# Optimization experiments

Measured on AMD Instinct MI355X. Metric: run time of the kernel, lower is better.

Reference implementation:

```python
import jax, jax.numpy as jnp
import numpy as np

N = 50_000          # nodes
E = 1_600_000       # edges (avg degree 32)
IN = 128            # in_feats
H = 4               # num_heads
F = 32              # out_feats per head
CUTOFF = 4.0        # bessel_cutoff
P = 7               # envelope_exponent + 1
ENV_A = -(P + 1) * (P + 2) / 2.0   # -36
ENV_B = P * (P + 2)                # 63
ENV_C = -P * (P + 1) / 2.0         # -28


def setup_inputs() -> dict:
    key = jax.random.key(0)
    ks = jax.random.split(key, 8)
    x = jax.random.normal(ks[0], (N, IN), dtype=jnp.float32)
    distance = jax.random.uniform(ks[1], (E,), dtype=jnp.float32) * CUTOFF
    W_src = jax.random.normal(ks[2], (H * F, IN), dtype=jnp.float32) * 0.05
    b_src = jnp.zeros((H * F,), dtype=jnp.float32)
    W_dst = jax.random.normal(ks[3], (H * F, IN), dtype=jnp.float32) * 0.05
    b_dst = jnp.zeros((H * F,), dtype=jnp.float32)
    attn = jax.random.normal(ks[4], (1, H, F), dtype=jnp.float32) * 0.1
    prelu_alpha = jnp.full((H,), 0.25, dtype=jnp.float32)
    frequencies = jnp.arange(1.0, H + 1.0, dtype=jnp.float32) * np.pi
    src = jax.random.randint(ks[5], (E,), 0, N, dtype=jnp.int32)
    dst = jax.random.randint(ks[6], (E,), 0, N, dtype=jnp.int32)
    return dict(x=x, distance=distance, W_src=W_src, b_src=b_src,
                W_dst=W_dst, b_dst=b_dst, attn=attn,
                prelu_alpha=prelu_alpha, frequencies=frequencies,
                src=src, dst=dst)


def _bessel_coeff(distance, frequencies):
    # distance: [E] -> d_scaled: [E,1]; frequencies: [H] -> coeff: [E,H]
    d = (distance / CUTOFF)[:, None]
    d_p0 = d ** P
    env = d + ENV_A * d_p0 + ENV_B * (d_p0 * d) + ENV_C * (d_p0 * d * d)
    return env * jnp.sin(frequencies * d)


def reference(x, distance, W_src, b_src, W_dst, b_dst, attn,
              prelu_alpha, frequencies, src, dst):
    n = x.shape[0]
    feat_src = (x @ W_src.T + b_src).reshape(n, H, F)   # [N,H,F]
    feat_dst = (x @ W_dst.T + b_dst).reshape(n, H, F)   # [N,H,F]

    coeff = _bessel_coeff(distance, frequencies)[:, :, None]  # [E,H,1]

    el = feat_src[src]                                  # [E,H,F] gather
    e = (el + feat_dst[dst]) * coeff                    # u_add_v then bessel scale
    e = jnp.where(e >= 0, e, prelu_alpha[None, :, None] * e)  # PReLU per head
    score = jnp.einsum('ehf,hf->eh', e, attn[0])        # [E,H]

    # edge softmax over incoming edges per dst node, per head
    seg_max = jax.ops.segment_max(score, dst, num_segments=n)        # [N,H]
    ex = jnp.exp(score - seg_max[dst])                               # [E,H]
    denom = jax.ops.segment_sum(ex, dst, num_segments=n)             # [N,H]
    a = ex / denom[dst]                                              # [E,H]

    # u_mul_e + scatter-sum aggregation
    msgs = el * a[:, :, None]                                        # [E,H,F]
    rst = jax.ops.segment_sum(msgs, dst, num_segments=n)             # [N,H,F]
    return rst
```

## Files before the change

### kernel.cpp

```cpp
#include <hip/hip_runtime.h>
#include <hip/hip_bf16.h>
#include <math.h>

#define N_NODES 50000
#define E_EDGES 1600000
#define HF 128
#define INV_CUTOFF 0.25f
#define ENV_A -36.0f
#define ENV_B 63.0f
#define ENV_C -28.0f

#define GEMM_BLOCKS ((N_NODES + 63) / 64)
#define REC_CAP 72
#define NBUCK 196
#define BUCK_CAP 8960
#define EPB 6250
#define SPLIT 4
#define LCAP 32

typedef __attribute__((ext_vector_type(8))) short bf16x8;
typedef __attribute__((ext_vector_type(4))) float f32x4;

__device__ __forceinline__ unsigned short f2bf(float f) {
  unsigned u = __float_as_uint(f);
  u += 0x7fffu + ((u >> 16) & 1u);
  return (unsigned short)(u >> 16);
}
__device__ __forceinline__ unsigned pack2(float lo, float hi) {
  return (unsigned)f2bf(lo) | ((unsigned)f2bf(hi) << 16);
}
__device__ __forceinline__ float2 up2(unsigned v) {
  return make_float2(__uint_as_float(v << 16), __uint_as_float(v & 0xffff0000u));
}

__device__ __forceinline__ float2 pk_add(float2 a, float2 b) {
  float2 d;
  asm("v_pk_add_f32 %0, %1, %2" : "=v"(d) : "v"(a), "v"(b));
  return d;
}
__device__ __forceinline__ float2 pk_fma(float2 a, float2 b, float2 c) {
  float2 d;
  asm("v_pk_fma_f32 %0, %1, %2, %3" : "=v"(d) : "v"(a), "v"(b), "v"(c));
  return d;
}
__device__ __forceinline__ float2 pk_abs(float2 a) {
  float2 d;
  d.x = __uint_as_float(__float_as_uint(a.x) & 0x7fffffffu);
  d.y = __uint_as_float(__float_as_uint(a.y) & 0x7fffffffu);
  return d;
}

__global__ void prep_w(const float* __restrict__ Ws, const float* __restrict__ Wd,
                       unsigned short* __restrict__ wbf) {
  const int q = blockIdx.x * 256 + threadIdx.x;
  if (q < 4096) {
    const int n = q >> 4, c = q & 15;
    const float* Wp = ((n < 128) ? Ws : Wd) + (size_t)(n & 127) * HF + c * 8;
    const float4 v0 = *(const float4*)Wp;
    const float4 v1 = *(const float4*)(Wp + 4);
    uint4 pk;
    pk.x = pack2(v0.x, v0.y); pk.y = pack2(v0.z, v0.w);
    pk.z = pack2(v1.x, v1.y); pk.w = pack2(v1.z, v1.w);
    *(uint4*)(wbf + (size_t)n * HF + ((c ^ (n & 15)) * 8)) = pk;
  }
}

__global__ __launch_bounds__(256) void feat_gemm(
    const float* __restrict__ x, const unsigned short* __restrict__ wbf,
    const float* __restrict__ bs, const float* __restrict__ bd,
    unsigned short* __restrict__ fs, float* __restrict__ fd) {
  __shared__ unsigned short wlds[256 * 128];

  for (int i = threadIdx.x; i < 4096; i += 256)
    ((uint4*)wlds)[i] = ((const uint4*)wbf)[i];

  const int lane = threadIdx.x & 63;
  const int wave = threadIdx.x >> 6;
  const int m = lane & 15;
  const int quad = lane >> 4;
  const int m0 = blockIdx.x * 64 + wave * 16;
  const int row = m0 + m;
  const int rowc = (row < N_NODES) ? row : (N_NODES - 1);

  union { bf16x8 v; unsigned u[4]; } af[4];
  #pragma unroll
  for (int kt = 0; kt < 4; kt++) {
    const float* xp = x + (size_t)rowc * HF + kt * 32 + quad * 8;
    const float4 u0 = *(const float4*)xp;
    const float4 u1 = *(const float4*)(xp + 4);
    af[kt].u[0] = pack2(u0.x, u0.y); af[kt].u[1] = pack2(u0.z, u0.w);
    af[kt].u[2] = pack2(u1.x, u1.y); af[kt].u[3] = pack2(u1.z, u1.w);
  }

  __syncthreads();

  float accA[16][4];
  #pragma unroll
  for (int nt = 0; nt < 16; nt++) {
    const int nrow = nt * 16 + m;
    f32x4 acc = {0.f, 0.f, 0.f, 0.f};
    #pragma unroll
    for (int kt = 0; kt < 4; kt++) {
      const int pc = (kt * 4 + quad) ^ m;
      const bf16x8 bf = *(const bf16x8*)(wlds + (size_t)nrow * HF + pc * 8);
      acc = __builtin_amdgcn_mfma_f32_16x16x32_bf16(af[kt].v, bf, acc, 0, 0, 0);
    }
    accA[nt][0] = acc[0]; accA[nt][1] = acc[1];
    accA[nt][2] = acc[2]; accA[nt][3] = acc[3];
  }

  __syncthreads();
  unsigned short* fsS = wlds;
  float* fdS = (float*)(wlds + 64 * 136);

  const int rl0 = wave * 16 + quad * 4;
  #pragma unroll
  for (int nt = 0; nt < 16; nt++) {
    const int col = nt * 16 + m;
    if (col < 128) {
      const float bias = bs[col];
      #pragma unroll
      for (int r = 0; r < 4; r++)
        fsS[(rl0 + r) * 136 + col] = f2bf(accA[nt][r] + bias);
    } else {
      const float bias = bd[col - 128];
      #pragma unroll
      for (int r = 0; r < 4; r++)
        fdS[(rl0 + r) * 132 + (col - 128)] = accA[nt][r] + bias;
    }
  }
  __syncthreads();

  for (int c = threadIdx.x; c < 1024; c += 256) {
    const int r = c >> 4, off = (c & 15) * 8;
    const int gr = blockIdx.x * 64 + r;
    if (gr < N_NODES)
      *(uint4*)(fs + (size_t)gr * HF + off) = *(const uint4*)(fsS + r * 136 + off);
  }
  for (int c = threadIdx.x; c < 2048; c += 256) {
    const int r = c >> 5, off = (c & 31) * 4;
    const int gr = blockIdx.x * 64 + r;
    if (gr < N_NODES)
      *(float4*)(fd + (size_t)gr * HF + off) = *(const float4*)(fdS + r * 132 + off);
  }
}

__global__ __launch_bounds__(256) void bucketize(
    const int* __restrict__ dst, const int* __restrict__ src,
    const float* __restrict__ dist,
    int* __restrict__ bcursor, unsigned* __restrict__ bb_pay,
    unsigned char* __restrict__ bb_loc) {
  __shared__ unsigned pay_s[EPB];
  __shared__ unsigned char bkt_s[EPB];
  __shared__ unsigned char loc_s[EPB];
  __shared__ int hist[NBUCK], loff[NBUCK], base[NBUCK], cur[NBUCK];
  for (int t = threadIdx.x; t < NBUCK; t += 256) { hist[t] = 0; cur[t] = 0; }
  __syncthreads();
  const int lo = blockIdx.x * EPB;
  for (int k = threadIdx.x; k < EPB; k += 256)
    atomicAdd(&hist[dst[lo + k] >> 8], 1);
  __syncthreads();
  if (threadIdx.x == 0) {
    int run = 0;
    for (int j = 0; j < NBUCK; j++) { loff[j] = run; run += hist[j]; }
  }
  __syncthreads();
  for (int t = threadIdx.x; t < NBUCK; t += 256)
    base[t] = atomicAdd(&bcursor[t], hist[t]);
  __syncthreads();
  for (int k = threadIdx.x; k < EPB; k += 256) {
    const int d = dst[lo + k];
    const int b = d >> 8;
    float ds = dist[lo + k] * (INV_CUTOFF * 65536.f);
    unsigned dq = (unsigned)(ds + 0.5f);
    if (dq > 65535u) dq = 65535u;
    const int s = loff[b] + atomicAdd(&cur[b], 1);
    pay_s[s] = (unsigned)src[lo + k] | (dq << 16);
    bkt_s[s] = (unsigned char)b;
    loc_s[s] = (unsigned char)(d & 255);
  }
  __syncthreads();
  for (int s = threadIdx.x; s < EPB; s += 256) {
    const int b = bkt_s[s];
    const int dest = base[b] + (s - loff[b]);
    if (dest < BUCK_CAP) {
      bb_pay[(size_t)b * BUCK_CAP + dest] = pay_s[s];
      bb_loc[(size_t)b * BUCK_CAP + dest] = loc_s[s];
    }
  }
}

__global__ __launch_bounds__(256) void bucket_scatter(
    const int* __restrict__ bcursor, const unsigned* __restrict__ bb_pay,
    const unsigned char* __restrict__ bb_loc,
    int* __restrict__ counts, unsigned* __restrict__ rec) {
  __shared__ int cnt[256];
  __shared__ unsigned recS[256 * LCAP];
  cnt[threadIdx.x] = 0;
  __syncthreads();
  const int b = blockIdx.x / SPLIT;
  const int q = blockIdx.x - b * SPLIT;
  const int total = min(bcursor[b], BUCK_CAP);
  const int lo = (total * q) / SPLIT;
  const int hi = (total * (q + 1)) / SPLIT;
  const size_t base = (size_t)b * BUCK_CAP;
  for (int i = lo + threadIdx.x; i < hi; i += 256) {
    const unsigned pay = bb_pay[base + i];
    const int local = bb_loc[base + i];
    const int r = atomicAdd(&cnt[local], 1);
    if (r < LCAP) recS[local * LCAP + r] = pay;
  }
  __syncthreads();
  const int node = (b << 8) + (int)threadIdx.x;
  if (node < N_NODES) {
    const int cl = min(cnt[threadIdx.x], LCAP);
    if (cl > 0) {
      const int gbase = atomicAdd(&counts[node], cl);
      unsigned* dstp = rec + (size_t)node * REC_CAP;
      const unsigned* srcp = recS + threadIdx.x * LCAP;
      for (int k = 0; k < cl; k++) {
        const int pos = gbase + k;
        if (pos < REC_CAP) dstp[pos] = srcp[k];
      }
    }
  }
}

__global__ __launch_bounds__(256) void gat_agg(
    const unsigned short* __restrict__ fs, const float* __restrict__ fd,
    const int* __restrict__ counts, const unsigned* __restrict__ rec,
    const float* __restrict__ attn, const float* __restrict__ alpha_p,
    const float* __restrict__ freqs, float* __restrict__ out) {
  const int wave = threadIdx.x >> 6;
  const int lane = threadIdx.x & 63;
  const int node = blockIdx.x * 4 + wave;
  if (node >= N_NODES) return;
  const int eslot = lane >> 4;
  const int h = (lane >> 2) & 3;
  const int j = lane & 3;
  const int fo = (h << 5) + (j << 3);

  int cnt = counts[node];
  cnt = (cnt < REC_CAP) ? cnt : REC_CAP;

  if (cnt <= 0) {
    if (eslot == 0) {
      float* o = out + (size_t)node * HF + fo;
      float4 z = {0.f, 0.f, 0.f, 0.f};
      *(float4*)o = z;
      *(float4*)(o + 4) = z;
    }
    return;
  }

  const float* fdp = fd + (size_t)node * HF + fo;
  const float2 f0 = *(const float2*)(fdp + 0);
  const float2 f1 = *(const float2*)(fdp + 2);
  const float2 f2 = *(const float2*)(fdp + 4);
  const float2 f3 = *(const float2*)(fdp + 6);
  const float2 t0 = *(const float2*)(attn + fo + 0);
  const float2 t1 = *(const float2*)(attn + fo + 2);
  const float2 t2 = *(const float2*)(attn + fo + 4);
  const float2 t3 = *(const float2*)(attn + fo + 6);
  const float al = alpha_p[h];
  const float c1 = 0.5f * (1.0f + al);
  const float c2 = 0.5f * (1.0f - al);
  const float fr = freqs[h];

  const int beg = node * REC_CAP;
  const int end = beg + cnt;
  const int last = end - 1;
  const unsigned short* fsp = fs + fo;

  int e0i = beg + eslot;
  unsigned rcur = rec[(e0i < end) ? e0i : last];
  uint4 ebcur = *(const uint4*)(fsp + ((size_t)(rcur & 0xffffu) << 7));
  int e1i = beg + 4 + eslot;
  unsigned rnext = rec[(e1i < end) ? e1i : last];

  float l = 0.f;
  float2 A0 = {0.f, 0.f}, A1 = {0.f, 0.f}, A2 = {0.f, 0.f}, A3 = {0.f, 0.f};

  for (int i = beg; i < end; i += 4) {
    const unsigned r = rcur;
    const uint4 eb = ebcur;
    rcur = rnext;
    const int inn = i + 8 + eslot;
    rnext = rec[(inn < end) ? inn : last];
    ebcur = *(const uint4*)(fsp + ((size_t)(rcur & 0xffffu) << 7));

    const bool valid = (i + eslot < end);
    const float d = (float)(r >> 16) * (1.0f / 65536.0f);
    const float2 e0 = up2(eb.x);
    const float2 e1 = up2(eb.y);
    const float2 e2 = up2(eb.z);
    const float2 e3 = up2(eb.w);

    const float d2 = d * d;
    const float d4 = d2 * d2;
    const float d7 = d4 * d2 * d;
    const float env = fmaf(d7, fmaf(d, fmaf(d, ENV_C, ENV_B), ENV_A), d);
    const float cf = env * __sinf(fr * d);
    const float k1 = c1 * cf;
    const float k2 = c2 * fabsf(cf);

    float2 D1 = {0.f, 0.f}, D2 = {0.f, 0.f};
    float2 u;
    u = pk_add(e0, f0); D1 = pk_fma(u, t0, D1); D2 = pk_fma(pk_abs(u), t0, D2);
    u = pk_add(e1, f1); D1 = pk_fma(u, t1, D1); D2 = pk_fma(pk_abs(u), t1, D2);
    u = pk_add(e2, f2); D1 = pk_fma(u, t2, D1); D2 = pk_fma(pk_abs(u), t2, D2);
    u = pk_add(e3, f3); D1 = pk_fma(u, t3, D1); D2 = pk_fma(pk_abs(u), t3, D2);

    float p = fmaf(k1, D1.x + D1.y, k2 * (D2.x + D2.y));
    p += __shfl_xor(p, 1);
    p += __shfl_xor(p, 2);

    const float w = valid ? __expf(p) : 0.f;
    l += w;
    const float2 w2 = {w, w};
    A0 = pk_fma(w2, e0, A0);
    A1 = pk_fma(w2, e1, A1);
    A2 = pk_fma(w2, e2, A2);
    A3 = pk_fma(w2, e3, A3);
  }

  #pragma unroll
  for (int mm = 16; mm < 64; mm <<= 1) {
    l    += __shfl_xor(l, mm);
    A0.x += __shfl_xor(A0.x, mm); A0.y += __shfl_xor(A0.y, mm);
    A1.x += __shfl_xor(A1.x, mm); A1.y += __shfl_xor(A1.y, mm);
    A2.x += __shfl_xor(A2.x, mm); A2.y += __shfl_xor(A2.y, mm);
    A3.x += __shfl_xor(A3.x, mm); A3.y += __shfl_xor(A3.y, mm);
  }

  if (eslot == 0) {
    const float rl = (l > 0.f) ? 1.0f / l : 0.f;
    float* o = out + (size_t)node * HF + fo;
    float4 o0 = {A0.x * rl, A0.y * rl, A1.x * rl, A1.y * rl};
    float4 o1 = {A2.x * rl, A2.y * rl, A3.x * rl, A3.y * rl};
    *(float4*)o = o0;
    *(float4*)(o + 4) = o1;
  }
}

extern "C" void kernel_launch(void* const* d_in, const int* in_sizes, int n_in,
                              void* d_out, int out_size, void* d_ws, size_t ws_size,
                              hipStream_t stream) {
  const float* x      = (const float*)d_in[0];
  const float* dist   = (const float*)d_in[1];
  const float* W_src  = (const float*)d_in[2];
  const float* b_src  = (const float*)d_in[3];
  const float* W_dst  = (const float*)d_in[4];
  const float* b_dst  = (const float*)d_in[5];
  const float* attn   = (const float*)d_in[6];
  const float* alpha  = (const float*)d_in[7];
  const float* freqs  = (const float*)d_in[8];
  const int*   src    = (const int*)d_in[9];
  const int*   dst    = (const int*)d_in[10];
  float* out = (float*)d_out;

  char* w = (char*)d_ws;
  size_t off = 0;
  auto alloc = [&](size_t bytes) -> void* {
    void* p = w + off;
    off += (bytes + 255) & ~(size_t)255;
    return p;
  };
  unsigned short* feat_src = (unsigned short*)alloc((size_t)N_NODES * HF * 2);
  float*          feat_dst = (float*)alloc((size_t)N_NODES * HF * 4);
  unsigned short* wbf      = (unsigned short*)alloc((size_t)256 * HF * 2);
  int*            counts   = (int*)alloc((size_t)N_NODES * 4);
  int*            bcursor  = (int*)alloc((size_t)NBUCK * 4);
  unsigned*       bb_pay   = (unsigned*)alloc((size_t)NBUCK * BUCK_CAP * 4);
  unsigned char*  bb_loc   = (unsigned char*)alloc((size_t)NBUCK * BUCK_CAP);
  unsigned*       rec      = (unsigned*)alloc((size_t)NBUCK * 256 * REC_CAP * 4);

  hipMemsetAsync(bcursor, 0, (size_t)NBUCK * 4, stream);
  hipMemsetAsync(counts, 0, (size_t)N_NODES * 4, stream);

  prep_w<<<16, 256, 0, stream>>>(W_src, W_dst, wbf);

  feat_gemm<<<GEMM_BLOCKS, 256, 0, stream>>>(x, wbf, b_src, b_dst, feat_src, feat_dst);

  bucketize<<<256, 256, 0, stream>>>(dst, src, dist, bcursor, bb_pay, bb_loc);

  bucket_scatter<<<NBUCK * SPLIT, 256, 0, stream>>>(bcursor, bb_pay, bb_loc, counts, rec);

  gat_agg<<<(N_NODES + 3) / 4, 256, 0, stream>>>(
      feat_src, feat_dst, counts, rec, attn, alpha, freqs, out);
}
```

Baseline: 253.0 us.

## Fold weight prep into GEMM, merge memsets, drop aggregation prefetch pipeline

Each GEMM block now converts the fp32 weights to swizzled bf16 itself, so the separate prep_w launch and its workspace buffer go away, and the two memsets become one over the contiguous counts and bcursor region. The aggregation kernel no longer has the early exit for zero-degree nodes or the software-pipelined prefetch of rec and feature rows. It loads them directly each iteration, which cuts register pressure but exposes gather latency. The rec buffer is also sized to the node count. Every GEMM block now repeats the fp32 weight read and conversion.

```diff
diff --git a/kernel.cpp b/kernel.cpp
--- a/kernel.cpp
+++ b/kernel.cpp
@@ -50,29 +50,23 @@
   return d;
 }
 
-__global__ void prep_w(const float* __restrict__ Ws, const float* __restrict__ Wd,
-                       unsigned short* __restrict__ wbf) {
-  const int q = blockIdx.x * 256 + threadIdx.x;
-  if (q < 4096) {
-    const int n = q >> 4, c = q & 15;
+__global__ __launch_bounds__(256) void feat_gemm(
+    const float* __restrict__ x, const float* __restrict__ Ws,
+    const float* __restrict__ Wd,
+    const float* __restrict__ bs, const float* __restrict__ bd,
+    unsigned short* __restrict__ fs, float* __restrict__ fd) {
+  __shared__ unsigned short wlds[256 * 128];
+
+  for (int i = threadIdx.x; i < 4096; i += 256) {
+    const int n = i >> 4, c = i & 15;
     const float* Wp = ((n < 128) ? Ws : Wd) + (size_t)(n & 127) * HF + c * 8;
     const float4 v0 = *(const float4*)Wp;
     const float4 v1 = *(const float4*)(Wp + 4);
     uint4 pk;
     pk.x = pack2(v0.x, v0.y); pk.y = pack2(v0.z, v0.w);
     pk.z = pack2(v1.x, v1.y); pk.w = pack2(v1.z, v1.w);
-    *(uint4*)(wbf + (size_t)n * HF + ((c ^ (n & 15)) * 8)) = pk;
-  }
-}
-
-__global__ __launch_bounds__(256) void feat_gemm(
-    const float* __restrict__ x, const unsigned short* __restrict__ wbf,
-    const float* __restrict__ bs, const float* __restrict__ bd,
-    unsigned short* __restrict__ fs, float* __restrict__ fd) {
-  __shared__ unsigned short wlds[256 * 128];
-
-  for (int i = threadIdx.x; i < 4096; i += 256)
-    ((uint4*)wlds)[i] = ((const uint4*)wbf)[i];
+    ((uint4*)wlds)[n * 16 + (c ^ (n & 15))] = pk;
+  }
 
   const int lane = threadIdx.x & 63;
   const int wave = threadIdx.x >> 6;
@@ -240,19 +234,6 @@
   const int j = lane & 3;
   const int fo = (h << 5) + (j << 3);
 
-  int cnt = counts[node];
-  cnt = (cnt < REC_CAP) ? cnt : REC_CAP;
-
-  if (cnt <= 0) {
-    if (eslot == 0) {
-      float* o = out + (size_t)node * HF + fo;
-      float4 z = {0.f, 0.f, 0.f, 0.f};
-      *(float4*)o = z;
-      *(float4*)(o + 4) = z;
-    }
-    return;
-  }
-
   const float* fdp = fd + (size_t)node * HF + fo;
   const float2 f0 = *(const float2*)(fdp + 0);
   const float2 f1 = *(const float2*)(fdp + 2);
@@ -268,29 +249,20 @@
   const float fr = freqs[h];
 
   const int beg = node * REC_CAP;
+  int cnt = counts[node];
+  cnt = (cnt < REC_CAP) ? cnt : REC_CAP;
   const int end = beg + cnt;
-  const int last = end - 1;
-  const unsigned short* fsp = fs + fo;
-
-  int e0i = beg + eslot;
-  unsigned rcur = rec[(e0i < end) ? e0i : last];
-  uint4 ebcur = *(const uint4*)(fsp + ((size_t)(rcur & 0xffffu) << 7));
-  int e1i = beg + 4 + eslot;
-  unsigned rnext = rec[(e1i < end) ? e1i : last];
 
   float l = 0.f;
   float2 A0 = {0.f, 0.f}, A1 = {0.f, 0.f}, A2 = {0.f, 0.f}, A3 = {0.f, 0.f};
 
   for (int i = beg; i < end; i += 4) {
-    const unsigned r = rcur;
-    const uint4 eb = ebcur;
-    rcur = rnext;
-    const int inn = i + 8 + eslot;
-    rnext = rec[(inn < end) ? inn : last];
-    ebcur = *(const uint4*)(fsp + ((size_t)(rcur & 0xffffu) << 7));
-
-    const bool valid = (i + eslot < end);
+    const int e = i + eslot;
+    const bool valid = (e < end);
+    const unsigned r = rec[valid ? e : beg];
+    const int s_idx = (int)(r & 0xffffu);
     const float d = (float)(r >> 16) * (1.0f / 65536.0f);
+    const uint4 eb = *(const uint4*)(fs + (size_t)s_idx * HF + fo);
     const float2 e0 = up2(eb.x);
     const float2 e1 = up2(eb.y);
     const float2 e2 = up2(eb.z);
@@ -368,19 +340,17 @@
   };
   unsigned short* feat_src = (unsigned short*)alloc((size_t)N_NODES * HF * 2);
   float*          feat_dst = (float*)alloc((size_t)N_NODES * HF * 4);
-  unsigned short* wbf      = (unsigned short*)alloc((size_t)256 * HF * 2);
   int*            counts   = (int*)alloc((size_t)N_NODES * 4);
   int*            bcursor  = (int*)alloc((size_t)NBUCK * 4);
   unsigned*       bb_pay   = (unsigned*)alloc((size_t)NBUCK * BUCK_CAP * 4);
   unsigned char*  bb_loc   = (unsigned char*)alloc((size_t)NBUCK * BUCK_CAP);
-  unsigned*       rec      = (unsigned*)alloc((size_t)NBUCK * 256 * REC_CAP * 4);
-
-  hipMemsetAsync(bcursor, 0, (size_t)NBUCK * 4, stream);
-  hipMemsetAsync(counts, 0, (size_t)N_NODES * 4, stream);
-
-  prep_w<<<16, 256, 0, stream>>>(W_src, W_dst, wbf);
-
-  feat_gemm<<<GEMM_BLOCKS, 256, 0, stream>>>(x, wbf, b_src, b_dst, feat_src, feat_dst);
+  unsigned*       rec      = (unsigned*)alloc((size_t)N_NODES * REC_CAP * 4);
+
+  const size_t counts_pad = ((size_t)N_NODES * 4 + 255) & ~(size_t)255;
+  hipMemsetAsync(counts, 0, counts_pad + (size_t)NBUCK * 4, stream);
+
+  feat_gemm<<<GEMM_BLOCKS, 256, 0, stream>>>(x, W_src, W_dst, b_src, b_dst,
+                                             feat_src, feat_dst);
 
   bucketize<<<256, 256, 0, stream>>>(dst, src, dist, bcursor, bb_pay, bb_loc);
 
```

After: 248.5 us. No clear change (-1.8%).
